# Kernel optimization log

Measured on AMD Instinct MI355X. Metric: run time of the kernel, lower is better.

The kernel has to match this reference:

```python
import jax, jax.numpy as jnp
import numpy as np

N_VEH = 40000
N_PATH = 400000
N_ACTOR = 128
N_MAP = 128
ACT_C = 32
PAT_C = 32
SIZE = N_ACTOR + N_MAP + ACT_C + PAT_C  # 320
HID = SIZE // 2  # 160
EPS = 1e-5


def _gn1(x, w, b):
    # GroupNorm with 1 group over channel dim of [N, C]: per-row normalize, per-channel affine
    mu = jnp.mean(x, axis=-1, keepdims=True)
    var = jnp.mean(jnp.square(x - mu), axis=-1, keepdims=True)
    return (x - mu) * jax.lax.rsqrt(var + EPS) * w + b


def setup_inputs() -> dict:
    key = jax.random.key(0)
    ks = jax.random.split(key, 12)
    inp = {
        "actors": jax.random.normal(ks[0], (N_VEH, N_ACTOR), jnp.float32),
        "paths": jax.random.normal(ks[1], (N_PATH, N_MAP), jnp.float32),
        "Z_act": jax.random.normal(ks[2], (N_VEH, ACT_C), jnp.float32),
        "Z_pat": jax.random.normal(ks[3], (N_PATH, PAT_C), jnp.float32),
        "u": jax.random.randint(ks[4], (N_PATH,), 0, N_VEH, jnp.int64 if jax.config.jax_enable_x64 else jnp.int32),
        # LinRes params (LaneGCN LinearRes: Linear(bias=False) -> GN -> ReLU -> Linear(bias=False) -> GN -> +transform(x) -> ReLU)
        "w1": jax.random.normal(ks[5], (HID, SIZE), jnp.float32) / np.sqrt(SIZE),
        "w2": jax.random.normal(ks[6], (HID, HID), jnp.float32) / np.sqrt(HID),
        "wt": jax.random.normal(ks[7], (HID, SIZE), jnp.float32) / np.sqrt(SIZE),
        "g1w": jnp.ones((HID,), jnp.float32),
        "g1b": jnp.zeros((HID,), jnp.float32),
        "g2w": jnp.ones((HID,), jnp.float32),
        "g2b": jnp.zeros((HID,), jnp.float32),
        # final head Linear(HID, 1)
        "wh": jax.random.normal(ks[8], (1, HID), jnp.float32) / np.sqrt(HID),
        "bh": jnp.zeros((1,), jnp.float32),
    }
    return inp


def reference(actors, paths, Z_act, Z_pat, u, w1, w2, wt, g1w, g1b, g2w, g2b, wh, bh):
    # edge-indexed gather + concat: [N_PATH, SIZE]
    x = jnp.concatenate([paths, Z_pat, actors[u], Z_act[u]], axis=-1)
    h = jnp.einsum('ns,hs->nh', x, w1)
    h = jax.nn.relu(_gn1(h, g1w, g1b))
    h = jnp.einsum('nh,gh->ng', h, w2)
    h = _gn1(h, g2w, g2b)
    h = jax.nn.relu(h + jnp.einsum('ns,hs->nh', x, wt))
    logits = jnp.einsum('nh,oh->no', h, wh) + bh
    return logits
```

## Files before the change

### kernel.cpp

```cpp
#include <hip/hip_runtime.h>
#include <hip/hip_bf16.h>

typedef short short8 __attribute__((ext_vector_type(8)));
typedef unsigned short ushortv8 __attribute__((ext_vector_type(8)));
typedef float floatx4 __attribute__((ext_vector_type(4)));

#define HP 168

__device__ __forceinline__ unsigned short f2bf(float f) {
    __hip_bfloat16 h = __float2bfloat16(f);
    return __builtin_bit_cast(unsigned short, h);
}
__device__ __forceinline__ float bf2f(unsigned short s) {
    __hip_bfloat16 h = __builtin_bit_cast(__hip_bfloat16, s);
    return __bfloat162float(h);
}

__device__ __forceinline__ float dpp_sum16(float v) {
    v += __builtin_bit_cast(float, __builtin_amdgcn_update_dpp(
             0, __builtin_bit_cast(int, v), 0x128, 0xF, 0xF, true));
    v += __builtin_bit_cast(float, __builtin_amdgcn_update_dpp(
             0, __builtin_bit_cast(int, v), 0x124, 0xF, 0xF, true));
    v += __builtin_bit_cast(float, __builtin_amdgcn_update_dpp(
             0, __builtin_bit_cast(int, v), 0x122, 0xF, 0xF, true));
    v += __builtin_bit_cast(float, __builtin_amdgcn_update_dpp(
             0, __builtin_bit_cast(int, v), 0x121, 0xF, 0xF, true));
    return v;
}

__global__ void pack_wc(const float* __restrict__ w1, const float* __restrict__ wt,
                        unsigned short* __restrict__ dst) {
    int i = blockIdx.x * 256 + threadIdx.x;
    if (i >= 320 * 320) return;
    int j = i & 7;
    int lane = (i >> 3) & 63;
    int r = i >> 9;
    int kb = r % 10;
    int t = r / 10;
    int n = t * 16 + (lane & 15);
    int k = kb * 32 + ((lane >> 4) << 3) + j;
    float v = (n < 160) ? w1[n * 320 + k] : wt[(n - 160) * 320 + k];
    dst[i] = f2bf(v);
}

__global__ void pack_w2(const float* __restrict__ w2, unsigned short* __restrict__ dst) {
    int i = blockIdx.x * 256 + threadIdx.x;
    if (i >= 160 * 160) return;
    int j = i & 7;
    int lane = (i >> 3) & 63;
    int r = i >> 9;
    int kb = r % 5;
    int t = r / 5;
    int n = t * 16 + (lane & 15);
    int k = kb * 32 + ((lane >> 4) << 3) + j;
    dst[i] = f2bf(w2[n * 160 + k]);
}

__global__ __launch_bounds__(128, 4) void fused_kernel(
    const float* __restrict__ actors, const float* __restrict__ paths,
    const float* __restrict__ Z_act, const float* __restrict__ Z_pat,
    const int* __restrict__ u,
    const unsigned short* __restrict__ pB1, const unsigned short* __restrict__ pB2,
    const float* __restrict__ g1w, const float* __restrict__ g1b,
    const float* __restrict__ g2w, const float* __restrict__ g2b,
    const float* __restrict__ wh, const float* __restrict__ bh,
    float* __restrict__ out)
{
    __shared__ __align__(16) char smem[20480];
    unsigned short* lX  = (unsigned short*)smem;
    unsigned short* lH1 = (unsigned short*)smem;
    unsigned short* lHT = (unsigned short*)(smem + 10752);
    float* sP  = (float*)(smem + 15872);
    float* sDp = (float*)(smem + 16384);

    const int tid  = threadIdx.x;
    const int wave = tid >> 6;
    const int lane = tid & 63;
    const int quad = lane >> 4;
    const int l15  = lane & 15;
    const int row0 = blockIdx.x * 32;

    float4 vD[5][2], vG[5][2];
    int uv[5], rr[5], qq[5];
    #pragma unroll
    for (int i = 0; i < 5; i++) {
        int f = i * 128 + tid;
        int r = f / 20, q = f - r * 20;
        rr[i] = r; qq[i] = q;
        const float* src = (q < 16) ? (paths + (size_t)(row0 + r) * 128 + q * 8)
                                    : (Z_pat + (size_t)(row0 + r) * 32 + (q - 16) * 8);
        vD[i][0] = *(const float4*)src;
        vD[i][1] = *(const float4*)(src + 4);
        uv[i] = u[row0 + r];
    }
    #pragma unroll
    for (int i = 0; i < 5; i++) {
        int q = qq[i];
        int un = uv[i];
        const float* src = (q < 16) ? (actors + (size_t)un * 128 + q * 8)
                                    : (Z_act + (size_t)un * 32 + (q - 16) * 8);
        vG[i][0] = *(const float4*)src;
        vG[i][1] = *(const float4*)(src + 4);
    }
    #pragma unroll
    for (int i = 0; i < 5; i++) {
        int r = rr[i], q = qq[i];
        int mt = r >> 4;
        {
            int kb = q >> 2, qd = q & 3;
            int slot = ((r & 15) | (qd << 4)) ^ ((qd ^ kb) & 7);
            ushortv8 sv;
            sv[0] = f2bf(vD[i][0].x); sv[1] = f2bf(vD[i][0].y);
            sv[2] = f2bf(vD[i][0].z); sv[3] = f2bf(vD[i][0].w);
            sv[4] = f2bf(vD[i][1].x); sv[5] = f2bf(vD[i][1].y);
            sv[6] = f2bf(vD[i][1].z); sv[7] = f2bf(vD[i][1].w);
            *(ushortv8*)(lX + ((mt * 10 + kb) * 64 + slot) * 8) = sv;
        }
        {
            int q8 = q + 20;
            int kb = q8 >> 2, qd = q8 & 3;
            int slot = ((r & 15) | (qd << 4)) ^ ((qd ^ kb) & 7);
            ushortv8 sv;
            sv[0] = f2bf(vG[i][0].x); sv[1] = f2bf(vG[i][0].y);
            sv[2] = f2bf(vG[i][0].z); sv[3] = f2bf(vG[i][0].w);
            sv[4] = f2bf(vG[i][1].x); sv[5] = f2bf(vG[i][1].y);
            sv[6] = f2bf(vG[i][1].z); sv[7] = f2bf(vG[i][1].w);
            *(ushortv8*)(lX + ((mt * 10 + kb) * 64 + slot) * 8) = sv;
        }
    }

    const unsigned short* pBw = pB1 + (size_t)wave * 51200 + (size_t)lane * 8;
    short8 ring[5];
    #pragma unroll
    for (int p = 0; p < 5; p++) {
        ring[p] = *(const short8*)(pBw + (size_t)(p * 10) * 512);
    }
    __syncthreads();

    floatx4 fzero = {0.f, 0.f, 0.f, 0.f};
    floatx4 acc[2][10];
    #pragma unroll
    for (int i = 0; i < 2; i++)
        #pragma unroll
        for (int j = 0; j < 10; j++) acc[i][j] = fzero;

    #pragma unroll
    for (int kb = 0; kb < 10; kb++) {
        int sl = (lane ^ ((quad ^ kb) & 7)) * 8;
        short8 a0 = *(const short8*)(lX + kb * 512 + sl);
        short8 a1 = *(const short8*)(lX + 5120 + kb * 512 + sl);
        #pragma unroll
        for (int ti = 0; ti < 10; ti++) {
            int p = kb * 10 + ti;
            short8 b = ring[p % 5];
            acc[0][ti] = __builtin_amdgcn_mfma_f32_16x16x32_bf16(a0, b, acc[0][ti], 0, 0, 0);
            acc[1][ti] = __builtin_amdgcn_mfma_f32_16x16x32_bf16(a1, b, acc[1][ti], 0, 0, 0);
            if (p + 5 < 100) {
                int p2 = p + 5, kb2 = p2 / 10, ti2 = p2 - kb2 * 10;
                ring[p2 % 5] = *(const short8*)(pBw + (size_t)(ti2 * 10 + kb2) * 512);
            }
        }
    }
    __syncthreads();

    ushort4 hk[2][5];
    if (wave == 0) {
        float mu_[2][4], rs_[2][4];
        #pragma unroll
        for (int mt = 0; mt < 2; mt++)
            #pragma unroll
            for (int r = 0; r < 4; r++) {
                float s = 0.f, q2 = 0.f;
                #pragma unroll
                for (int ti = 0; ti < 10; ti++) {
                    float v = acc[mt][ti][r];
                    s += v; q2 += v * v;
                }
                s = dpp_sum16(s); q2 = dpp_sum16(q2);
                float mu = s * (1.f / 160.f);
                float var = q2 * (1.f / 160.f) - mu * mu;
                mu_[mt][r] = mu;
                rs_[mt][r] = rsqrtf(var + 1e-5f);
            }
        float gw[10], gb[10];
        #pragma unroll
        for (int ti = 0; ti < 10; ti++) {
            int n = ti * 16 + l15;
            gw[ti] = g1w[n]; gb[ti] = g1b[n];
        }
        #pragma unroll
        for (int mt = 0; mt < 2; mt++)
            #pragma unroll
            for (int ti = 0; ti < 10; ti++)
                #pragma unroll
                for (int r = 0; r < 4; r++) {
                    float v = (acc[mt][ti][r] - mu_[mt][r]) * rs_[mt][r] * gw[ti] + gb[ti];
                    v = fmaxf(v, 0.f);
                    lH1[(mt * 16 + quad * 4 + r) * HP + ti * 16 + l15] = f2bf(v);
                }
    } else {
        #pragma unroll
        for (int mt = 0; mt < 2; mt++)
            #pragma unroll
            for (int tk = 0; tk < 5; tk++) {
                ushort4 kv;
                kv.x = f2bf(acc[mt][tk + 5][0]); kv.y = f2bf(acc[mt][tk + 5][1]);
                kv.z = f2bf(acc[mt][tk + 5][2]); kv.w = f2bf(acc[mt][tk + 5][3]);
                hk[mt][tk] = kv;
                ushort4 sv;
                sv.x = f2bf(acc[mt][tk][0]); sv.y = f2bf(acc[mt][tk][1]);
                sv.z = f2bf(acc[mt][tk][2]); sv.w = f2bf(acc[mt][tk][3]);
                int ch = tk * 16 + l15;
                int rg = (mt * 4 + quad) ^ (l15 & 7);
                *(ushort4*)(lHT + (ch * 8 + rg) * 4) = sv;
            }
    }

    const unsigned short* pB2w = pB2 + (size_t)wave * 12800 + (size_t)lane * 8;
    short8 ring2[4];
    #pragma unroll
    for (int p = 0; p < 4; p++) {
        ring2[p] = *(const short8*)(pB2w + (size_t)(p * 5) * 512);
    }
    __syncthreads();

    floatx4 acc2[2][5];
    #pragma unroll
    for (int i = 0; i < 2; i++)
        #pragma unroll
        for (int j = 0; j < 5; j++) acc2[i][j] = fzero;

    #pragma unroll
    for (int kb = 0; kb < 5; kb++) {
        short8 a0 = *(const short8*)(lH1 + l15 * HP + kb * 32 + quad * 8);
        short8 a1 = *(const short8*)(lH1 + (16 + l15) * HP + kb * 32 + quad * 8);
        #pragma unroll
        for (int ti = 0; ti < 5; ti++) {
            int p = kb * 5 + ti;
            short8 b = ring2[p % 4];
            acc2[0][ti] = __builtin_amdgcn_mfma_f32_16x16x32_bf16(a0, b, acc2[0][ti], 0, 0, 0);
            acc2[1][ti] = __builtin_amdgcn_mfma_f32_16x16x32_bf16(a1, b, acc2[1][ti], 0, 0, 0);
            if (p + 4 < 25) {
                int p2 = p + 4, kb2 = p2 / 5, ti2 = p2 - kb2 * 5;
                ring2[p2 % 4] = *(const short8*)(pB2w + (size_t)(ti2 * 5 + kb2) * 512);
            }
        }
    }

    #pragma unroll
    for (int mt = 0; mt < 2; mt++)
        #pragma unroll
        for (int r = 0; r < 4; r++) {
            float s = 0.f, q2 = 0.f;
            #pragma unroll
            for (int ti = 0; ti < 5; ti++) {
                float v = acc2[mt][ti][r];
                s += v; q2 += v * v;
            }
            s = dpp_sum16(s); q2 = dpp_sum16(q2);
            if (l15 == 0) {
                int m = mt * 16 + quad * 4 + r;
                float2 pv; pv.x = s; pv.y = q2;
                *(float2*)(sP + m * 4 + wave * 2) = pv;
            }
        }
    __syncthreads();

    float mu2_[2][4], rs2_[2][4];
    #pragma unroll
    for (int mt = 0; mt < 2; mt++)
        #pragma unroll
        for (int r = 0; r < 4; r++) {
            int m = mt * 16 + quad * 4 + r;
            float4 pv = *(const float4*)(sP + m * 4);
            float ts = pv.x + pv.z;
            float tq = pv.y + pv.w;
            float mu = ts * (1.f / 160.f);
            float var = tq * (1.f / 160.f) - mu * mu;
            mu2_[mt][r] = mu;
            rs2_[mt][r] = rsqrtf(var + 1e-5f);
        }

    {
        float g2wv[5], g2bv[5], whv[5];
        #pragma unroll
        for (int ti = 0; ti < 5; ti++) {
            int n = wave * 80 + ti * 16 + l15;
            g2wv[ti] = g2w[n]; g2bv[ti] = g2b[n]; whv[ti] = wh[n];
        }
        float dp[8];
        #pragma unroll
        for (int k = 0; k < 8; k++) dp[k] = 0.f;

        #pragma unroll
        for (int mt = 0; mt < 2; mt++)
            #pragma unroll
            for (int ti = 0; ti < 5; ti++) {
                ushort4 hv;
                if (wave == 0) {
                    int ch = ti * 16 + l15;
                    int rg = (mt * 4 + quad) ^ (l15 & 7);
                    hv = *(const ushort4*)(lHT + (ch * 8 + rg) * 4);
                } else {
                    hv = hk[mt][ti];
                }
                float hvf[4];
                hvf[0] = bf2f(hv.x); hvf[1] = bf2f(hv.y);
                hvf[2] = bf2f(hv.z); hvf[3] = bf2f(hv.w);
                #pragma unroll
                for (int r = 0; r < 4; r++) {
                    float v = (acc2[mt][ti][r] - mu2_[mt][r]) * rs2_[mt][r] * g2wv[ti] + g2bv[ti];
                    v += hvf[r];
                    v = fmaxf(v, 0.f);
                    dp[mt * 4 + r] += v * whv[ti];
                }
            }
        #pragma unroll
        for (int k = 0; k < 8; k++) dp[k] = dpp_sum16(dp[k]);
        if (l15 == 0) {
            #pragma unroll
            for (int mt = 0; mt < 2; mt++)
                #pragma unroll
                for (int r = 0; r < 4; r++) {
                    int m = mt * 16 + quad * 4 + r;
                    sDp[m * 2 + wave] = dp[mt * 4 + r];
                }
        }
    }
    __syncthreads();
    if (tid < 32) {
        float2 d = *(const float2*)(sDp + tid * 2);
        out[row0 + tid] = d.x + d.y + bh[0];
    }
}

extern "C" void kernel_launch(void* const* d_in, const int* in_sizes, int n_in,
                              void* d_out, int out_size, void* d_ws, size_t ws_size,
                              hipStream_t stream) {
    const float* actors = (const float*)d_in[0];
    const float* paths  = (const float*)d_in[1];
    const float* Z_act  = (const float*)d_in[2];
    const float* Z_pat  = (const float*)d_in[3];
    const int*   u      = (const int*)d_in[4];
    const float* w1     = (const float*)d_in[5];
    const float* w2     = (const float*)d_in[6];
    const float* wt     = (const float*)d_in[7];
    const float* g1w    = (const float*)d_in[8];
    const float* g1b    = (const float*)d_in[9];
    const float* g2w    = (const float*)d_in[10];
    const float* g2b    = (const float*)d_in[11];
    const float* wh     = (const float*)d_in[12];
    const float* bh     = (const float*)d_in[13];
    float* out = (float*)d_out;

    unsigned short* pB1 = (unsigned short*)d_ws;
    unsigned short* pB2 = pB1 + 320 * 320;

    hipLaunchKernelGGL(pack_wc, dim3(400), dim3(256), 0, stream, w1, wt, pB1);
    hipLaunchKernelGGL(pack_w2, dim3(100), dim3(256), 0, stream, w2, pB2);
    hipLaunchKernelGGL(fused_kernel, dim3(400000 / 32), dim3(128), 0, stream,
                       actors, paths, Z_act, Z_pat, u, pB1, pB2,
                       g1w, g1b, g2w, g2b, wh, bh, out);
}
```

Baseline: 566.2 us.

## Split fused LinRes kernel over 8 waves with 64-row tiles

Each block now handles 64 rows with 512 threads (8 waves) instead of 32 rows with 2 waves. Each wave computes a 32x80 tile of the first GEMM and a 16x80 tile of the second. The first GroupNorm is now reduced through shared-memory partial sums across waves, and weight fragments are double-buffered with a two-step prefetch. The aim is more parallelism per row and less per-wave register and accumulator pressure, at the cost of more barriers, 40KB of LDS per block and narrower float4 gather loads.

```diff
diff --git a/kernel.cpp b/kernel.cpp
--- a/kernel.cpp
+++ b/kernel.cpp
@@ -2,7 +2,6 @@
 #include <hip/hip_bf16.h>
 
 typedef short short8 __attribute__((ext_vector_type(8)));
-typedef unsigned short ushortv8 __attribute__((ext_vector_type(8)));
 typedef float floatx4 __attribute__((ext_vector_type(4)));
 
 #define HP 168
@@ -56,7 +55,7 @@
     dst[i] = f2bf(w2[n * 160 + k]);
 }
 
-__global__ __launch_bounds__(128, 4) void fused_kernel(
+__global__ __launch_bounds__(512, 4) void fused_kernel(
     const float* __restrict__ actors, const float* __restrict__ paths,
     const float* __restrict__ Z_act, const float* __restrict__ Z_pat,
     const int* __restrict__ u,
@@ -66,272 +65,271 @@
     const float* __restrict__ wh, const float* __restrict__ bh,
     float* __restrict__ out)
 {
-    __shared__ __align__(16) char smem[20480];
+    __shared__ __align__(16) char smem[40960];
     unsigned short* lX  = (unsigned short*)smem;
     unsigned short* lH1 = (unsigned short*)smem;
-    unsigned short* lHT = (unsigned short*)(smem + 10752);
-    float* sP  = (float*)(smem + 15872);
-    float* sDp = (float*)(smem + 16384);
+    unsigned short* lHT = (unsigned short*)(smem + 21504);
+    float2* sP  = (float2*)(smem + 31744);
+    float*  sDp = (float*)(smem + 32768);
 
     const int tid  = threadIdx.x;
-    const int wave = tid >> 6;
+    const int w    = tid >> 6;
     const int lane = tid & 63;
     const int quad = lane >> 4;
     const int l15  = lane & 15;
-    const int row0 = blockIdx.x * 32;
-
-    float4 vD[5][2], vG[5][2];
+    const int row0 = blockIdx.x * 64;
+
+    const int wm1 = w & 1;
+    const int wn1 = w >> 1;
+    const int nh  = (w >> 1) & 1;
+    const int mq  = (w & 1) * 2 + ((w < 4) ? (1 - (w >> 1)) : ((w >> 1) - 2));
+
+    float4 vD[5], vG[5];
     int uv[5], rr[5], qq[5];
     #pragma unroll
     for (int i = 0; i < 5; i++) {
-        int f = i * 128 + tid;
-        int r = f / 20, q = f - r * 20;
-        rr[i] = r; qq[i] = q;
-        const float* src = (q < 16) ? (paths + (size_t)(row0 + r) * 128 + q * 8)
-                                    : (Z_pat + (size_t)(row0 + r) * 32 + (q - 16) * 8);
-        vD[i][0] = *(const float4*)src;
-        vD[i][1] = *(const float4*)(src + 4);
+        int f = i * 512 + tid;
+        int r = f / 40, sq = f - r * 40;
+        rr[i] = r; qq[i] = sq;
+        const float* src = (sq < 32) ? (paths + (size_t)(row0 + r) * 128 + sq * 4)
+                                     : (Z_pat + (size_t)(row0 + r) * 32 + (sq - 32) * 4);
+        vD[i] = *(const float4*)src;
         uv[i] = u[row0 + r];
     }
     #pragma unroll
     for (int i = 0; i < 5; i++) {
-        int q = qq[i];
+        int sq = qq[i];
         int un = uv[i];
-        const float* src = (q < 16) ? (actors + (size_t)un * 128 + q * 8)
-                                    : (Z_act + (size_t)un * 32 + (q - 16) * 8);
-        vG[i][0] = *(const float4*)src;
-        vG[i][1] = *(const float4*)(src + 4);
+        const float* src = (sq < 32) ? (actors + (size_t)un * 128 + sq * 4)
+                                     : (Z_act + (size_t)un * 32 + (sq - 32) * 4);
+        vG[i] = *(const float4*)src;
     }
     #pragma unroll
     for (int i = 0; i < 5; i++) {
-        int r = rr[i], q = qq[i];
+        int r = rr[i], sq = qq[i];
         int mt = r >> 4;
+        int g = sq >> 1, h = sq & 1;
         {
-            int kb = q >> 2, qd = q & 3;
+            int kb = g >> 2, qd = g & 3;
             int slot = ((r & 15) | (qd << 4)) ^ ((qd ^ kb) & 7);
-            ushortv8 sv;
-            sv[0] = f2bf(vD[i][0].x); sv[1] = f2bf(vD[i][0].y);
-            sv[2] = f2bf(vD[i][0].z); sv[3] = f2bf(vD[i][0].w);
-            sv[4] = f2bf(vD[i][1].x); sv[5] = f2bf(vD[i][1].y);
-            sv[6] = f2bf(vD[i][1].z); sv[7] = f2bf(vD[i][1].w);
-            *(ushortv8*)(lX + ((mt * 10 + kb) * 64 + slot) * 8) = sv;
+            ushort4 sv;
+            sv.x = f2bf(vD[i].x); sv.y = f2bf(vD[i].y);
+            sv.z = f2bf(vD[i].z); sv.w = f2bf(vD[i].w);
+            *(ushort4*)(lX + ((mt * 10 + kb) * 64 + slot) * 8 + h * 4) = sv;
         }
         {
-            int q8 = q + 20;
-            int kb = q8 >> 2, qd = q8 & 3;
+            int g8 = g + 20;
+            int kb = g8 >> 2, qd = g8 & 3;
             int slot = ((r & 15) | (qd << 4)) ^ ((qd ^ kb) & 7);
-            ushortv8 sv;
-            sv[0] = f2bf(vG[i][0].x); sv[1] = f2bf(vG[i][0].y);
-            sv[2] = f2bf(vG[i][0].z); sv[3] = f2bf(vG[i][0].w);
-            sv[4] = f2bf(vG[i][1].x); sv[5] = f2bf(vG[i][1].y);
-            sv[6] = f2bf(vG[i][1].z); sv[7] = f2bf(vG[i][1].w);
-            *(ushortv8*)(lX + ((mt * 10 + kb) * 64 + slot) * 8) = sv;
-        }
-    }
-
-    const unsigned short* pBw = pB1 + (size_t)wave * 51200 + (size_t)lane * 8;
-    short8 ring[5];
-    #pragma unroll
-    for (int p = 0; p < 5; p++) {
-        ring[p] = *(const short8*)(pBw + (size_t)(p * 10) * 512);
+            ushort4 sv;
+            sv.x = f2bf(vG[i].x); sv.y = f2bf(vG[i].y);
+            sv.z = f2bf(vG[i].z); sv.w = f2bf(vG[i].w);
+            *(ushort4*)(lX + ((mt * 10 + kb) * 64 + slot) * 8 + h * 4) = sv;
+        }
+    }
+
+    const unsigned short* pBw = pB1 + (size_t)wn1 * 25600 + (size_t)lane * 8;
+    short8 bA[5], bB[5];
+    #pragma unroll
+    for (int ti = 0; ti < 5; ti++) {
+        bA[ti] = *(const short8*)(pBw + (size_t)(ti * 10 + 0) * 512);
+        bB[ti] = *(const short8*)(pBw + (size_t)(ti * 10 + 1) * 512);
     }
     __syncthreads();
 
     floatx4 fzero = {0.f, 0.f, 0.f, 0.f};
-    floatx4 acc[2][10];
+    floatx4 acc[2][5];
     #pragma unroll
     for (int i = 0; i < 2; i++)
         #pragma unroll
-        for (int j = 0; j < 10; j++) acc[i][j] = fzero;
+        for (int j = 0; j < 5; j++) acc[i][j] = fzero;
 
     #pragma unroll
     for (int kb = 0; kb < 10; kb++) {
         int sl = (lane ^ ((quad ^ kb) & 7)) * 8;
-        short8 a0 = *(const short8*)(lX + kb * 512 + sl);
-        short8 a1 = *(const short8*)(lX + 5120 + kb * 512 + sl);
-        #pragma unroll
-        for (int ti = 0; ti < 10; ti++) {
-            int p = kb * 10 + ti;
-            short8 b = ring[p % 5];
-            acc[0][ti] = __builtin_amdgcn_mfma_f32_16x16x32_bf16(a0, b, acc[0][ti], 0, 0, 0);
-            acc[1][ti] = __builtin_amdgcn_mfma_f32_16x16x32_bf16(a1, b, acc[1][ti], 0, 0, 0);
-            if (p + 5 < 100) {
-                int p2 = p + 5, kb2 = p2 / 10, ti2 = p2 - kb2 * 10;
-                ring[p2 % 5] = *(const short8*)(pBw + (size_t)(ti2 * 10 + kb2) * 512);
-            }
-        }
-    }
-    __syncthreads();
-
-    ushort4 hk[2][5];
-    if (wave == 0) {
-        float mu_[2][4], rs_[2][4];
+        short8 a0 = *(const short8*)(lX + ((wm1 * 2 + 0) * 10 + kb) * 512 + sl);
+        short8 a1 = *(const short8*)(lX + ((wm1 * 2 + 1) * 10 + kb) * 512 + sl);
+        short8 bN[5];
+        if (kb + 2 < 10) {
+            #pragma unroll
+            for (int ti = 0; ti < 5; ti++)
+                bN[ti] = *(const short8*)(pBw + (size_t)(ti * 10 + kb + 2) * 512);
+        }
+        #pragma unroll
+        for (int ti = 0; ti < 5; ti++) {
+            acc[0][ti] = __builtin_amdgcn_mfma_f32_16x16x32_bf16(a0, bA[ti], acc[0][ti], 0, 0, 0);
+            acc[1][ti] = __builtin_amdgcn_mfma_f32_16x16x32_bf16(a1, bA[ti], acc[1][ti], 0, 0, 0);
+        }
+        #pragma unroll
+        for (int ti = 0; ti < 5; ti++) { bA[ti] = bB[ti]; bB[ti] = bN[ti]; }
+    }
+    __syncthreads();
+
+    ushort4 hk[5];
+    if (w >= 4) {
+        int mt_keep = wn1 - 2;
+        int mt_store = 1 - mt_keep;
+        int grp = w - 4;
+        #pragma unroll
+        for (int ti = 0; ti < 5; ti++) {
+            ushort4 kv;
+            kv.x = f2bf(acc[mt_keep][ti][0]); kv.y = f2bf(acc[mt_keep][ti][1]);
+            kv.z = f2bf(acc[mt_keep][ti][2]); kv.w = f2bf(acc[mt_keep][ti][3]);
+            hk[ti] = kv;
+            ushort4 sv;
+            sv.x = f2bf(acc[mt_store][ti][0]); sv.y = f2bf(acc[mt_store][ti][1]);
+            sv.z = f2bf(acc[mt_store][ti][2]); sv.w = f2bf(acc[mt_store][ti][3]);
+            int idx = (grp * 80 + ti * 16 + l15) * 4 + quad;
+            *(ushort4*)(lHT + idx * 4) = sv;
+        }
+    } else {
         #pragma unroll
         for (int mt = 0; mt < 2; mt++)
             #pragma unroll
             for (int r = 0; r < 4; r++) {
                 float s = 0.f, q2 = 0.f;
                 #pragma unroll
-                for (int ti = 0; ti < 10; ti++) {
+                for (int ti = 0; ti < 5; ti++) {
                     float v = acc[mt][ti][r];
                     s += v; q2 += v * v;
                 }
                 s = dpp_sum16(s); q2 = dpp_sum16(q2);
-                float mu = s * (1.f / 160.f);
-                float var = q2 * (1.f / 160.f) - mu * mu;
-                mu_[mt][r] = mu;
-                rs_[mt][r] = rsqrtf(var + 1e-5f);
-            }
-        float gw[10], gb[10];
-        #pragma unroll
-        for (int ti = 0; ti < 10; ti++) {
-            int n = ti * 16 + l15;
+                if (l15 == 0) {
+                    int row = wm1 * 32 + mt * 16 + quad * 4 + r;
+                    float2 pv; pv.x = s; pv.y = q2;
+                    sP[wn1 * 64 + row] = pv;
+                }
+            }
+    }
+    __syncthreads();
+
+    const unsigned short* pB2w = pB2 + (size_t)nh * 12800 + (size_t)lane * 8;
+    short8 b2A[5], b2B[5];
+    #pragma unroll
+    for (int ti = 0; ti < 5; ti++) {
+        b2A[ti] = *(const short8*)(pB2w + (size_t)(ti * 5 + 0) * 512);
+        b2B[ti] = *(const short8*)(pB2w + (size_t)(ti * 5 + 1) * 512);
+    }
+
+    if (w < 4) {
+        float gw[5], gb[5];
+        #pragma unroll
+        for (int ti = 0; ti < 5; ti++) {
+            int n = wn1 * 80 + ti * 16 + l15;
             gw[ti] = g1w[n]; gb[ti] = g1b[n];
         }
         #pragma unroll
         for (int mt = 0; mt < 2; mt++)
             #pragma unroll
-            for (int ti = 0; ti < 10; ti++)
+            for (int r = 0; r < 4; r++) {
+                int row = wm1 * 32 + mt * 16 + quad * 4 + r;
+                float2 p0 = sP[row];
+                float2 p1 = sP[64 + row];
+                float mu = (p0.x + p1.x) * (1.f / 160.f);
+                float var = (p0.y + p1.y) * (1.f / 160.f) - mu * mu;
+                float rs = rsqrtf(var + 1e-5f);
                 #pragma unroll
-                for (int r = 0; r < 4; r++) {
-                    float v = (acc[mt][ti][r] - mu_[mt][r]) * rs_[mt][r] * gw[ti] + gb[ti];
+                for (int ti = 0; ti < 5; ti++) {
+                    float v = (acc[mt][ti][r] - mu) * rs * gw[ti] + gb[ti];
                     v = fmaxf(v, 0.f);
-                    lH1[(mt * 16 + quad * 4 + r) * HP + ti * 16 + l15] = f2bf(v);
+                    lH1[row * HP + wn1 * 80 + ti * 16 + l15] = f2bf(v);
                 }
-    } else {
-        #pragma unroll
-        for (int mt = 0; mt < 2; mt++)
-            #pragma unroll
-            for (int tk = 0; tk < 5; tk++) {
-                ushort4 kv;
-                kv.x = f2bf(acc[mt][tk + 5][0]); kv.y = f2bf(acc[mt][tk + 5][1]);
-                kv.z = f2bf(acc[mt][tk + 5][2]); kv.w = f2bf(acc[mt][tk + 5][3]);
-                hk[mt][tk] = kv;
-                ushort4 sv;
-                sv.x = f2bf(acc[mt][tk][0]); sv.y = f2bf(acc[mt][tk][1]);
-                sv.z = f2bf(acc[mt][tk][2]); sv.w = f2bf(acc[mt][tk][3]);
-                int ch = tk * 16 + l15;
-                int rg = (mt * 4 + quad) ^ (l15 & 7);
-                *(ushort4*)(lHT + (ch * 8 + rg) * 4) = sv;
-            }
-    }
-
-    const unsigned short* pB2w = pB2 + (size_t)wave * 12800 + (size_t)lane * 8;
-    short8 ring2[4];
-    #pragma unroll
-    for (int p = 0; p < 4; p++) {
-        ring2[p] = *(const short8*)(pB2w + (size_t)(p * 5) * 512);
-    }
-    __syncthreads();
-
-    floatx4 acc2[2][5];
-    #pragma unroll
-    for (int i = 0; i < 2; i++)
-        #pragma unroll
-        for (int j = 0; j < 5; j++) acc2[i][j] = fzero;
+            }
+    }
+    __syncthreads();
+
+    floatx4 acc2[5];
+    #pragma unroll
+    for (int j = 0; j < 5; j++) acc2[j] = fzero;
 
     #pragma unroll
     for (int kb = 0; kb < 5; kb++) {
-        short8 a0 = *(const short8*)(lH1 + l15 * HP + kb * 32 + quad * 8);
-        short8 a1 = *(const short8*)(lH1 + (16 + l15) * HP + kb * 32 + quad * 8);
-        #pragma unroll
-        for (int ti = 0; ti < 5; ti++) {
-            int p = kb * 5 + ti;
-            short8 b = ring2[p % 4];
-            acc2[0][ti] = __builtin_amdgcn_mfma_f32_16x16x32_bf16(a0, b, acc2[0][ti], 0, 0, 0);
-            acc2[1][ti] = __builtin_amdgcn_mfma_f32_16x16x32_bf16(a1, b, acc2[1][ti], 0, 0, 0);
-            if (p + 4 < 25) {
-                int p2 = p + 4, kb2 = p2 / 5, ti2 = p2 - kb2 * 5;
-                ring2[p2 % 4] = *(const short8*)(pB2w + (size_t)(ti2 * 5 + kb2) * 512);
-            }
-        }
-    }
-
-    #pragma unroll
-    for (int mt = 0; mt < 2; mt++)
+        short8 a = *(const short8*)(lH1 + (mq * 16 + l15) * HP + kb * 32 + quad * 8);
+        short8 bN[5];
+        if (kb + 2 < 5) {
+            #pragma unroll
+            for (int ti = 0; ti < 5; ti++)
+                bN[ti] = *(const short8*)(pB2w + (size_t)(ti * 5 + kb + 2) * 512);
+        }
+        #pragma unroll
+        for (int ti = 0; ti < 5; ti++)
+            acc2[ti] = __builtin_amdgcn_mfma_f32_16x16x32_bf16(a, b2A[ti], acc2[ti], 0, 0, 0);
+        #pragma unroll
+        for (int ti = 0; ti < 5; ti++) { b2A[ti] = b2B[ti]; b2B[ti] = bN[ti]; }
+    }
+
+    #pragma unroll
+    for (int r = 0; r < 4; r++) {
+        float s = 0.f, q2 = 0.f;
+        #pragma unroll
+        for (int ti = 0; ti < 5; ti++) {
+            float v = acc2[ti][r];
+            s += v; q2 += v * v;
+        }
+        s = dpp_sum16(s); q2 = dpp_sum16(q2);
+        if (l15 == 0) {
+            int row = mq * 16 + quad * 4 + r;
+            float2 pv; pv.x = s; pv.y = q2;
+            sP[nh * 64 + row] = pv;
+        }
+    }
+    __syncthreads();
+
+    {
+        float mu2[4], rs2[4];
         #pragma unroll
         for (int r = 0; r < 4; r++) {
-            float s = 0.f, q2 = 0.f;
-            #pragma unroll
-            for (int ti = 0; ti < 5; ti++) {
-                float v = acc2[mt][ti][r];
-                s += v; q2 += v * v;
-            }
-            s = dpp_sum16(s); q2 = dpp_sum16(q2);
-            if (l15 == 0) {
-                int m = mt * 16 + quad * 4 + r;
-                float2 pv; pv.x = s; pv.y = q2;
-                *(float2*)(sP + m * 4 + wave * 2) = pv;
-            }
-        }
-    __syncthreads();
-
-    float mu2_[2][4], rs2_[2][4];
-    #pragma unroll
-    for (int mt = 0; mt < 2; mt++)
-        #pragma unroll
-        for (int r = 0; r < 4; r++) {
-            int m = mt * 16 + quad * 4 + r;
-            float4 pv = *(const float4*)(sP + m * 4);
-            float ts = pv.x + pv.z;
-            float tq = pv.y + pv.w;
-            float mu = ts * (1.f / 160.f);
-            float var = tq * (1.f / 160.f) - mu * mu;
-            mu2_[mt][r] = mu;
-            rs2_[mt][r] = rsqrtf(var + 1e-5f);
-        }
-
-    {
+            int row = mq * 16 + quad * 4 + r;
+            float2 p0 = sP[row];
+            float2 p1 = sP[64 + row];
+            float mu = (p0.x + p1.x) * (1.f / 160.f);
+            float var = (p0.y + p1.y) * (1.f / 160.f) - mu * mu;
+            mu2[r] = mu;
+            rs2[r] = rsqrtf(var + 1e-5f);
+        }
         float g2wv[5], g2bv[5], whv[5];
         #pragma unroll
         for (int ti = 0; ti < 5; ti++) {
-            int n = wave * 80 + ti * 16 + l15;
+            int n = nh * 80 + ti * 16 + l15;
             g2wv[ti] = g2w[n]; g2bv[ti] = g2b[n]; whv[ti] = wh[n];
         }
-        float dp[8];
-        #pragma unroll
-        for (int k = 0; k < 8; k++) dp[k] = 0.f;
-
-        #pragma unroll
-        for (int mt = 0; mt < 2; mt++)
-            #pragma unroll
-            for (int ti = 0; ti < 5; ti++) {
-                ushort4 hv;
-                if (wave == 0) {
-                    int ch = ti * 16 + l15;
-                    int rg = (mt * 4 + quad) ^ (l15 & 7);
-                    hv = *(const ushort4*)(lHT + (ch * 8 + rg) * 4);
-                } else {
-                    hv = hk[mt][ti];
-                }
-                float hvf[4];
-                hvf[0] = bf2f(hv.x); hvf[1] = bf2f(hv.y);
-                hvf[2] = bf2f(hv.z); hvf[3] = bf2f(hv.w);
-                #pragma unroll
-                for (int r = 0; r < 4; r++) {
-                    float v = (acc2[mt][ti][r] - mu2_[mt][r]) * rs2_[mt][r] * g2wv[ti] + g2bv[ti];
-                    v += hvf[r];
-                    v = fmaxf(v, 0.f);
-                    dp[mt * 4 + r] += v * whv[ti];
-                }
-            }
-        #pragma unroll
-        for (int k = 0; k < 8; k++) dp[k] = dpp_sum16(dp[k]);
+        float dp[4];
+        #pragma unroll
+        for (int r = 0; r < 4; r++) dp[r] = 0.f;
+
+        int grp = nh * 2 + wm1;
+        #pragma unroll
+        for (int ti = 0; ti < 5; ti++) {
+            ushort4 hv;
+            if (w >= 4) {
+                hv = hk[ti];
+            } else {
+                int idx = (grp * 80 + ti * 16 + l15) * 4 + quad;
+                hv = *(const ushort4*)(lHT + idx * 4);
+            }
+            float hvf[4];
+            hvf[0] = bf2f(hv.x); hvf[1] = bf2f(hv.y);
+            hvf[2] = bf2f(hv.z); hvf[3] = bf2f(hv.w);
+            #pragma unroll
+            for (int r = 0; r < 4; r++) {
+                float v = (acc2[ti][r] - mu2[r]) * rs2[r] * g2wv[ti] + g2bv[ti];
+                v += hvf[r];
+                v = fmaxf(v, 0.f);
+                dp[r] += v * whv[ti];
+            }
+        }
+        #pragma unroll
+        for (int r = 0; r < 4; r++) dp[r] = dpp_sum16(dp[r]);
         if (l15 == 0) {
             #pragma unroll
-            for (int mt = 0; mt < 2; mt++)
-                #pragma unroll
-                for (int r = 0; r < 4; r++) {
-                    int m = mt * 16 + quad * 4 + r;
-                    sDp[m * 2 + wave] = dp[mt * 4 + r];
-                }
-        }
-    }
-    __syncthreads();
-    if (tid < 32) {
-        float2 d = *(const float2*)(sDp + tid * 2);
-        out[row0 + tid] = d.x + d.y + bh[0];
-    }
+            for (int r = 0; r < 4; r++) {
+                int row = mq * 16 + quad * 4 + r;
+                sDp[nh * 64 + row] = dp[r];
+            }
+        }
+    }
+    __syncthreads();
+    if (tid < 64) out[row0 + tid] = sDp[tid] + sDp[64 + tid] + bh[0];
 }
 
 extern "C" void kernel_launch(void* const* d_in, const int* in_sizes, int n_in,
@@ -358,7 +356,7 @@
 
     hipLaunchKernelGGL(pack_wc, dim3(400), dim3(256), 0, stream, w1, wt, pB1);
     hipLaunchKernelGGL(pack_w2, dim3(100), dim3(256), 0, stream, w2, pB2);
-    hipLaunchKernelGGL(fused_kernel, dim3(400000 / 32), dim3(128), 0, stream,
+    hipLaunchKernelGGL(fused_kernel, dim3(400000 / 64), dim3(512), 0, stream,
                        actors, paths, Z_act, Z_pat, u, pB1, pB2,
                        g1w, g1b, g2w, g2b, wh, bh, out);
 }
```

New measurement: 852.8 us. 1.51x slower.
